# Performance work log

Measured on AMD Instinct MI355X. Metric: run time of the kernel, lower is better.

The kernel has to match this reference:

```python
import jax, jax.numpy as jnp
import numpy as np

N = 100_000      # nodes
E = 1_600_000    # edges
G = 256          # graphs in batch
FIN = 128


def setup_inputs() -> dict:
    key = jax.random.key(0)
    ks = jax.random.split(key, 12)
    inp = {
        "x": jax.random.normal(ks[0], (N, FIN), dtype=jnp.float32),
        "edge_index": jax.random.randint(ks[1], (2, E), 0, N),
        "batch": jnp.sort(jax.random.randint(ks[2], (N,), 0, G)),
    }
    def lin(k, fi, fo):
        return jax.random.normal(k, (fi, fo), dtype=jnp.float32) / np.sqrt(fi)
    inp["W1"], inp["b1"] = lin(ks[3], 128, 128), jnp.zeros((128,), jnp.float32)
    inp["W2"], inp["b2"] = lin(ks[4], 128, 128), jnp.zeros((128,), jnp.float32)
    inp["W3"], inp["b3"] = lin(ks[5], 128, 128), jnp.zeros((128,), jnp.float32)
    inp["Wa1"], inp["ba1"] = lin(ks[6], 128, 64), jnp.zeros((64,), jnp.float32)
    inp["Wa2"], inp["ba2"] = lin(ks[7], 64, 32), jnp.zeros((32,), jnp.float32)
    inp["Wa3"], inp["ba3"] = lin(ks[8], 32, 1), jnp.zeros((1,), jnp.float32)
    inp["Wm1"], inp["bm1"] = lin(ks[9], 128, 128), jnp.zeros((128,), jnp.float32)
    inp["Wm2"], inp["bm2"] = lin(ks[10], 128, 256), jnp.zeros((256,), jnp.float32)
    return inp


def _gcn_norm(edge_index, n):
    # PyG gcn_norm with added self-loops: D^{-1/2}(A+I)D^{-1/2}
    loops = jnp.arange(n)
    row = jnp.concatenate([edge_index[0], loops])
    col = jnp.concatenate([edge_index[1], loops])
    deg = jax.ops.segment_sum(jnp.ones_like(col, dtype=jnp.float32), col, n)
    dinv = jnp.where(deg > 0, jax.lax.rsqrt(jnp.maximum(deg, 1.0)), 0.0)
    return row, col, dinv[row] * dinv[col]


def _gcn(x, row, col, norm, W, b, n):
    h = x @ W                                   # linear first, then propagate
    out = jax.ops.segment_sum(h[row] * norm[:, None], col, n)
    return out + b


def _seg_softmax(w, batch, g):
    m = jax.ops.segment_max(w, batch, g)        # [G, 1]
    m = jnp.where(jnp.isfinite(m), m, 0.0)      # guard empty segments
    e = jnp.exp(w - m[batch])
    s = jax.ops.segment_sum(e, batch, g)
    return e / (s[batch] + 1e-16)


def reference(x, edge_index, batch, W1, b1, W2, b2, W3, b3,
              Wa1, ba1, Wa2, ba2, Wa3, ba3, Wm1, bm1, Wm2, bm2):
    n = x.shape[0]
    row, col, norm = _gcn_norm(edge_index, n)
    x = jax.nn.relu(_gcn(x, row, col, norm, W1, b1, n))
    x = jax.nn.relu(_gcn(x, row, col, norm, W2, b2, n))
    x = jax.nn.relu(_gcn(x, row, col, norm, W3, b3, n))
    w = jax.nn.relu(_gcn(x, row, col, norm, Wa1, ba1, n))
    w = jax.nn.relu(_gcn(w, row, col, norm, Wa2, ba2, n))
    w = jax.nn.relu(_gcn(w, row, col, norm, Wa3, ba3, n))  # [N, 1]
    w = _seg_softmax(w, batch, G)
    pooled = jax.ops.segment_sum(x * w, batch, G)           # [G, 128]
    h = jax.nn.relu(pooled @ Wm1 + bm1)
    return h @ Wm2 + bm2                                    # [G, 256]
```

## Files before the change

kernel.cpp:

```cpp
#include <hip/hip_runtime.h>
#include <hip/hip_bf16.h>

struct f4 { float x, y, z, w; };
__device__ __forceinline__ f4 ld4(const float* p) { return *(const f4*)p; }
__device__ __forceinline__ void st4(float* p, f4 v) { *(f4*)p = v; }
__device__ __forceinline__ void acc4(f4& a, f4 b) { a.x += b.x; a.y += b.y; a.z += b.z; a.w += b.w; }


__global__ void count_kernel(const int* __restrict__ col, int* __restrict__ cnt, int E) {
    int i = blockIdx.x * 256 + threadIdx.x;
    int e0 = i * 4;
    if (e0 + 4 <= E) {
        int4 c = *(const int4*)(col + e0);
        atomicAdd(&cnt[c.x], 1);
        atomicAdd(&cnt[c.y], 1);
        atomicAdd(&cnt[c.z], 1);
        atomicAdd(&cnt[c.w], 1);
    } else {
        for (int e = e0; e < E; ++e) atomicAdd(&cnt[col[e]], 1);
    }
}


__global__ void scan1_kernel(const int* __restrict__ cnt, int* __restrict__ bsum, int n) {
    __shared__ int red[256];
    int t = threadIdx.x;
    int i = blockIdx.x * 256 + t;
    red[t] = (i < n) ? cnt[i] : 0;
    __syncthreads();
    for (int off = 128; off > 0; off >>= 1) {
        if (t < off) red[t] += red[t + off];
        __syncthreads();
    }
    if (t == 0) bsum[blockIdx.x] = red[0];
}

__global__ void scan2_kernel(int* __restrict__ bsum, int nb) {
    __shared__ int s[1024];
    int t = threadIdx.x;
    int v = (t < nb) ? bsum[t] : 0;
    s[t] = v;
    __syncthreads();
    for (int off = 1; off < 1024; off <<= 1) {
        int u = (t >= off) ? s[t - off] : 0;
        __syncthreads();
        s[t] += u;
        __syncthreads();
    }
    if (t < nb) bsum[t] = s[t] - v;
}

__global__ void scan3_kernel(const int* __restrict__ cnt, const int* __restrict__ bsum,
                             int* __restrict__ ptr, int n) {
    __shared__ int s[256];
    int t = threadIdx.x;
    int i = blockIdx.x * 256 + t;
    int v = (i < n) ? cnt[i] : 0;
    s[t] = v;
    __syncthreads();
    for (int off = 1; off < 256; off <<= 1) {
        int u = (t >= off) ? s[t - off] : 0;
        __syncthreads();
        s[t] += u;
        __syncthreads();
    }
    int excl = s[t] - v + bsum[blockIdx.x];
    if (i < n) ptr[i] = excl;
    if (i == n - 1) ptr[n] = excl + v;
}

__global__ void dinv_fill_kernel(const int* __restrict__ cnt, const int* __restrict__ ptr,
                                 float* __restrict__ dinv, int* __restrict__ fillp, int n) {
    int i = blockIdx.x * 256 + threadIdx.x;
    if (i >= n) return;
    dinv[i] = rsqrtf((float)(cnt[i] + 1));
    fillp[i] = ptr[i];
}

__global__ void fill_kernel(const int* __restrict__ row, const int* __restrict__ col,
                            int* __restrict__ fillp, int* __restrict__ csr_row, int E) {
    int i = blockIdx.x * 256 + threadIdx.x;
    int e0 = i * 4;
    if (e0 + 4 <= E) {
        int4 c = *(const int4*)(col + e0);
        int4 r = *(const int4*)(row + e0);
        int p0 = atomicAdd(&fillp[c.x], 1);
        int p1 = atomicAdd(&fillp[c.y], 1);
        int p2 = atomicAdd(&fillp[c.z], 1);
        int p3 = atomicAdd(&fillp[c.w], 1);
        csr_row[p0] = r.x; csr_row[p1] = r.y; csr_row[p2] = r.z; csr_row[p3] = r.w;
    } else {
        for (int e = e0; e < E; ++e) {
            int p = atomicAdd(&fillp[col[e]], 1);
            csr_row[p] = row[e];
        }
    }
}


template<int K, int FOUT>
__global__ __launch_bounds__(256) void gemm_kernel(const float* __restrict__ A,
                            const float* __restrict__ W, const float* __restrict__ scale,
                            float* __restrict__ C, int n) {
    constexpr int ROWS = 64;
    constexpr int NCG = FOUT / 4;
    constexpr int RG  = 256 / NCG;
    constexpr int RPT = ROWS / RG;
    __shared__ float As[ROWS * K];
    int t = threadIdx.x;
    int r0 = blockIdx.x * ROWS;
    for (int i = t; i < ROWS * K / 4; i += 256) {
        int idx = i * 4;
        int r = r0 + idx / K;
        f4 v;
        if (r < n) v = ld4(A + (size_t)r0 * K + idx);
        else { v.x = v.y = v.z = v.w = 0.f; }
        st4(As + idx, v);
    }
    __syncthreads();
    int cg = t % NCG, rg = t / NCG;
    int c = cg * 4, rb = rg * RPT;
    f4 acc[RPT];
#pragma unroll
    for (int i = 0; i < RPT; ++i) { acc[i].x = acc[i].y = acc[i].z = acc[i].w = 0.f; }
    for (int k = 0; k < K; k += 4) {
        f4 w0 = ld4(W + (size_t)(k + 0) * FOUT + c);
        f4 w1 = ld4(W + (size_t)(k + 1) * FOUT + c);
        f4 w2 = ld4(W + (size_t)(k + 2) * FOUT + c);
        f4 w3 = ld4(W + (size_t)(k + 3) * FOUT + c);
#pragma unroll
        for (int i = 0; i < RPT; ++i) {
            f4 a = ld4(As + (rb + i) * K + k);
            acc[i].x += a.x * w0.x + a.y * w1.x + a.z * w2.x + a.w * w3.x;
            acc[i].y += a.x * w0.y + a.y * w1.y + a.z * w2.y + a.w * w3.y;
            acc[i].z += a.x * w0.z + a.y * w1.z + a.z * w2.z + a.w * w3.z;
            acc[i].w += a.x * w0.w + a.y * w1.w + a.z * w2.w + a.w * w3.w;
        }
    }
#pragma unroll
    for (int i = 0; i < RPT; ++i) {
        int r = r0 + rb + i;
        if (r < n) {
            float s = scale[r];
            f4 v = acc[i];
            v.x *= s; v.y *= s; v.z *= s; v.w *= s;
            st4(C + (size_t)r * FOUT + c, v);
        }
    }
}


template<int K, int FOUT, bool WRITE_AGG>
__global__ __launch_bounds__(512, 4) void propgemm_kernel(const float* __restrict__ Hs,
                            const int* __restrict__ ptr, const int* __restrict__ rows,
                            const float* __restrict__ dinv, const float* __restrict__ bias,
                            const float* __restrict__ W, float* __restrict__ aggout,
                            float* __restrict__ C, int n) {
    constexpr int ROWS = 64;
    constexpr int BT = 512;
    __shared__ float As[ROWS * K];
    int t = threadIdx.x;
    int r0 = blockIdx.x * ROWS;

    constexpr int L = K / 4;
    constexpr int NPB = BT / L;
    int q = t % L, ln = t / L;
    const int f4i = q * 4;
    for (int p = 0; p < ROWS; p += NPB) {
        int node = r0 + p + ln;
        f4 a0;
        if (node < n) {
            a0 = ld4(Hs + (size_t)node * K + f4i);
            f4 a1, a2, a3;
            a1.x = a1.y = a1.z = a1.w = 0.f; a2 = a1; a3 = a1;
            int e0 = ptr[node], e1 = ptr[node + 1];
            int e = e0;
            for (; e + 4 <= e1; e += 4) {
                int rr0 = rows[e], rr1 = rows[e+1], rr2 = rows[e+2], rr3 = rows[e+3];
                acc4(a0, ld4(Hs + (size_t)rr0 * K + f4i));
                acc4(a1, ld4(Hs + (size_t)rr1 * K + f4i));
                acc4(a2, ld4(Hs + (size_t)rr2 * K + f4i));
                acc4(a3, ld4(Hs + (size_t)rr3 * K + f4i));
            }
            for (; e < e1; ++e) acc4(a0, ld4(Hs + (size_t)rows[e] * K + f4i));
            acc4(a0, a1); acc4(a2, a3); acc4(a0, a2);
            float dn = dinv[node];
            f4 b = ld4(bias + f4i);
            a0.x = fmaxf(a0.x * dn + b.x, 0.f);
            a0.y = fmaxf(a0.y * dn + b.y, 0.f);
            a0.z = fmaxf(a0.z * dn + b.z, 0.f);
            a0.w = fmaxf(a0.w * dn + b.w, 0.f);
            if (WRITE_AGG) st4(aggout + (size_t)node * K + f4i, a0);
        } else { a0.x = a0.y = a0.z = a0.w = 0.f; }
        st4(As + (p + ln) * K + f4i, a0);
    }
    __syncthreads();

    constexpr int NCG = FOUT / 4;
    constexpr int RG  = BT / NCG;
    constexpr int RPT = ROWS / RG;
    int cg = t % NCG, rg = t / NCG;
    int c = cg * 4, rb = rg * RPT;
    f4 acc[RPT];
#pragma unroll
    for (int i = 0; i < RPT; ++i) { acc[i].x = acc[i].y = acc[i].z = acc[i].w = 0.f; }
    for (int k = 0; k < K; k += 4) {
        f4 w0 = ld4(W + (size_t)(k + 0) * FOUT + c);
        f4 w1 = ld4(W + (size_t)(k + 1) * FOUT + c);
        f4 w2 = ld4(W + (size_t)(k + 2) * FOUT + c);
        f4 w3 = ld4(W + (size_t)(k + 3) * FOUT + c);
#pragma unroll
        for (int i = 0; i < RPT; ++i) {
            f4 a = ld4(As + (rb + i) * K + k);
            acc[i].x += a.x * w0.x + a.y * w1.x + a.z * w2.x + a.w * w3.x;
            acc[i].y += a.x * w0.y + a.y * w1.y + a.z * w2.y + a.w * w3.y;
            acc[i].z += a.x * w0.z + a.y * w1.z + a.z * w2.z + a.w * w3.z;
            acc[i].w += a.x * w0.w + a.y * w1.w + a.z * w2.w + a.w * w3.w;
        }
    }
#pragma unroll
    for (int i = 0; i < RPT; ++i) {
        int r = r0 + rb + i;
        if (r < n) {
            float s = dinv[r];
            f4 v = acc[i];
            v.x *= s; v.y *= s; v.z *= s; v.w *= s;
            st4(C + (size_t)r * FOUT + c, v);
        }
    }
}


__global__ __launch_bounds__(256) void propdot_kernel(const float* __restrict__ Hs,
                            const int* __restrict__ ptr, const int* __restrict__ rows,
                            const float* __restrict__ dinv, const float* __restrict__ bias,
                            const float* __restrict__ W, float* __restrict__ outv, int n) {
    int t = threadIdx.x;
    int q = t & 7;
    int ln = t >> 3;
    int node = blockIdx.x * 32 + ln;
    if (node >= n) return;
    const int f4i = q * 4;
    f4 a0 = ld4(Hs + (size_t)node * 32 + f4i);
    f4 a1, a2, a3;
    a1.x = a1.y = a1.z = a1.w = 0.f; a2 = a1; a3 = a1;
    int e0 = ptr[node], e1 = ptr[node + 1];
    int e = e0;
    for (; e + 4 <= e1; e += 4) {
        int rr0 = rows[e], rr1 = rows[e+1], rr2 = rows[e+2], rr3 = rows[e+3];
        acc4(a0, ld4(Hs + (size_t)rr0 * 32 + f4i));
        acc4(a1, ld4(Hs + (size_t)rr1 * 32 + f4i));
        acc4(a2, ld4(Hs + (size_t)rr2 * 32 + f4i));
        acc4(a3, ld4(Hs + (size_t)rr3 * 32 + f4i));
    }
    for (; e < e1; ++e) acc4(a0, ld4(Hs + (size_t)rows[e] * 32 + f4i));
    acc4(a0, a1); acc4(a2, a3); acc4(a0, a2);
    float dn = dinv[node];
    f4 b = ld4(bias + f4i);
    float vx = fmaxf(a0.x * dn + b.x, 0.f);
    float vy = fmaxf(a0.y * dn + b.y, 0.f);
    float vz = fmaxf(a0.z * dn + b.z, 0.f);
    float vw = fmaxf(a0.w * dn + b.w, 0.f);
    f4 w = ld4(W + f4i);
    float part = vx * w.x + vy * w.y + vz * w.z + vw * w.w;
    part += __shfl_down(part, 4, 8);
    part += __shfl_down(part, 2, 8);
    part += __shfl_down(part, 1, 8);
    if (q == 0) outv[node] = part * dn;
}

__global__ void prop1_kernel(const float* __restrict__ Hs, const int* __restrict__ ptr,
                             const int* __restrict__ rows, const float* __restrict__ dinv,
                             const float* __restrict__ bias, float* __restrict__ out, int n) {
    int node = blockIdx.x * 256 + threadIdx.x;
    if (node >= n) return;
    float a0 = Hs[node], a1 = 0.f, a2 = 0.f, a3 = 0.f;
    int e0 = ptr[node], e1 = ptr[node + 1];
    int e = e0;
    for (; e + 4 <= e1; e += 4) {
        a0 += Hs[rows[e]];
        a1 += Hs[rows[e+1]];
        a2 += Hs[rows[e+2]];
        a3 += Hs[rows[e+3]];
    }
    for (; e < e1; ++e) a0 += Hs[rows[e]];
    float v = (a0 + a1 + a2 + a3) * dinv[node] + bias[0];
    out[node] = v > 0.f ? v : 0.f;
}


__global__ void bounds_kernel(const int* __restrict__ batch, int* __restrict__ start,
                              int n, int g_cnt) {
    int g = blockIdx.x * 256 + threadIdx.x;
    if (g > g_cnt) return;
    if (g == g_cnt) { start[g] = n; return; }
    int lo = 0, hi = n;
    while (lo < hi) { int mid = (lo + hi) >> 1; if (batch[mid] < g) lo = mid + 1; else hi = mid; }
    start[g] = lo;
}

__global__ __launch_bounds__(256) void softpool_kernel(const float* __restrict__ x,
                              const float* __restrict__ w, const int* __restrict__ start,
                              float* __restrict__ pooled) {
    int g = blockIdx.x;
    int s = start[g], e = start[g + 1];
    int t = threadIdx.x;
    __shared__ float red[256];
    float mx = -1e30f;
    for (int i = s + t; i < e; i += 256) mx = fmaxf(mx, w[i]);
    red[t] = mx; __syncthreads();
    for (int off = 128; off > 0; off >>= 1) {
        if (t < off) red[t] = fmaxf(red[t], red[t + off]);
        __syncthreads();
    }
    float m = (e > s) ? red[0] : 0.f;
    __syncthreads();
    float sm = 0.f;
    for (int i = s + t; i < e; i += 256) sm += expf(w[i] - m);
    red[t] = sm; __syncthreads();
    for (int off = 128; off > 0; off >>= 1) {
        if (t < off) red[t] += red[t + off];
        __syncthreads();
    }
    float denom = red[0] + 1e-16f;
    __syncthreads();
    int f = t & 127;
    int half = t >> 7;
    float acc = 0.f;
    for (int i = s + half; i < e; i += 2)
        acc += x[(size_t)i * 128 + f] * (expf(w[i] - m) / denom);
    red[t] = acc; __syncthreads();
    if (half == 0) pooled[g * 128 + f] = red[f] + red[128 + f];
}


__global__ void mlp1_kernel(const float* __restrict__ pooled, const float* __restrict__ Wm1,
                            const float* __restrict__ bm1, float* __restrict__ hidden) {
    int g = blockIdx.x, j = threadIdx.x;
    __shared__ float p[128];
    p[j] = pooled[g * 128 + j];
    __syncthreads();
    float acc = bm1[j];
    for (int k = 0; k < 128; ++k) acc += p[k] * Wm1[k * 128 + j];
    hidden[g * 128 + j] = acc > 0.f ? acc : 0.f;
}

__global__ void mlp2_kernel(const float* __restrict__ hidden, const float* __restrict__ Wm2,
                            const float* __restrict__ bm2, float* __restrict__ out) {
    int g = blockIdx.x, j = threadIdx.x;
    __shared__ float h[128];
    if (j < 128) h[j] = hidden[g * 128 + j];
    __syncthreads();
    float acc = bm2[j];
    for (int k = 0; k < 128; ++k) acc += h[k] * Wm2[k * 256 + j];
    out[g * 256 + j] = acc;
}


extern "C" void kernel_launch(void* const* d_in, const int* in_sizes, int n_in,
                              void* d_out, int out_size, void* d_ws, size_t ws_size,
                              hipStream_t stream) {
    const float* x    = (const float*)d_in[0];
    const int*   ei   = (const int*)d_in[1];
    const int*   batch= (const int*)d_in[2];
    const float* W1 = (const float*)d_in[3];  const float* b1 = (const float*)d_in[4];
    const float* W2 = (const float*)d_in[5];  const float* b2 = (const float*)d_in[6];
    const float* W3 = (const float*)d_in[7];  const float* b3 = (const float*)d_in[8];
    const float* Wa1= (const float*)d_in[9];  const float* ba1= (const float*)d_in[10];
    const float* Wa2= (const float*)d_in[11]; const float* ba2= (const float*)d_in[12];
    const float* Wa3= (const float*)d_in[13]; const float* ba3= (const float*)d_in[14];
    const float* Wm1= (const float*)d_in[15]; const float* bm1= (const float*)d_in[16];
    const float* Wm2= (const float*)d_in[17]; const float* bm2= (const float*)d_in[18];
    float* out = (float*)d_out;

    const int N = in_sizes[0] / 128;
    const int E = in_sizes[1] / 2;
    const int G = out_size / 256;

    const int* row = ei;
    const int* col = ei + E;

    char* wp = (char*)d_ws;
    auto alloc = [&](size_t bytes) {
        void* p = wp;
        wp += (bytes + 255) & ~(size_t)255;
        return p;
    };
    const int NB256 = (N + 255) / 256;
    int*   cnt     = (int*)alloc((size_t)N * 4);
    int*   ptr     = (int*)alloc((size_t)(N + 1) * 4);
    int*   bsum    = (int*)alloc((size_t)NB256 * 4);
    int*   fillp   = (int*)alloc((size_t)N * 4);
    int*   csr_row = (int*)alloc((size_t)E * 4);
    float* dinv    = (float*)alloc((size_t)N * 4);
    float* bufA    = (float*)alloc((size_t)N * 128 * 4);
    float* bufB    = (float*)alloc((size_t)N * 128 * 4);
    float* a64_lin = (float*)alloc((size_t)N * 64 * 4);
    float* a32_lin = (float*)alloc((size_t)N * 32 * 4);
    float* wb0     = (float*)alloc((size_t)N * 4);
    float* wb1     = (float*)alloc((size_t)N * 4);
    int*   gstart  = (int*)alloc((size_t)(G + 1) * 4);
    float* pooled  = (float*)alloc((size_t)G * 128 * 4);
    float* hidden  = (float*)alloc((size_t)G * 128 * 4);

    hipMemsetAsync(cnt, 0, (size_t)N * 4, stream);

    const int E4B = ((E + 3) / 4 + 255) / 256;
    const int NB = NB256;

    count_kernel<<<E4B, 256, 0, stream>>>(col, cnt, E);
    scan1_kernel<<<NB, 256, 0, stream>>>(cnt, bsum, N);
    scan2_kernel<<<1, 1024, 0, stream>>>(bsum, NB);
    scan3_kernel<<<NB, 256, 0, stream>>>(cnt, bsum, ptr, N);
    dinv_fill_kernel<<<NB, 256, 0, stream>>>(cnt, ptr, dinv, fillp, N);
    fill_kernel<<<E4B, 256, 0, stream>>>(row, col, fillp, csr_row, E);
    bounds_kernel<<<(G + 256) / 256, 256, 0, stream>>>(batch, gstart, N, G);

    const int GB64 = (N + 63) / 64;

    gemm_kernel<128,128><<<GB64, 256, 0, stream>>>(x, W1, dinv, bufA, N);
    propgemm_kernel<128,128,false><<<GB64, 512, 0, stream>>>(bufA, ptr, csr_row, dinv, b1, W2, nullptr, bufB, N);
    propgemm_kernel<128,128,false><<<GB64, 512, 0, stream>>>(bufB, ptr, csr_row, dinv, b2, W3, nullptr, bufA, N);
    propgemm_kernel<128,64,true><<<GB64, 512, 0, stream>>>(bufA, ptr, csr_row, dinv, b3, Wa1, bufB, a64_lin, N);
    propgemm_kernel<64,32,false><<<GB64, 512, 0, stream>>>(a64_lin, ptr, csr_row, dinv, ba1, Wa2, nullptr, a32_lin, N);
    propdot_kernel<<<(N + 31) / 32, 256, 0, stream>>>(a32_lin, ptr, csr_row, dinv, ba2, Wa3, wb0, N);
    prop1_kernel<<<NB, 256, 0, stream>>>(wb0, ptr, csr_row, dinv, ba3, wb1, N);

    softpool_kernel<<<G, 256, 0, stream>>>(bufB, wb1, gstart, pooled);

    mlp1_kernel<<<G, 128, 0, stream>>>(pooled, Wm1, bm1, hidden);
    mlp2_kernel<<<G, 256, 0, stream>>>(hidden, Wm2, bm2, out);
}
```

Measured before the change: 1.146 ms.

## Fuse scan with dinv init, merge MLP kernels, shrink propgemm blocks

Folds the dinv/fillp initialization into the final scan kernel and merges the two MLP head kernels into one, removing two launches and an intermediate buffer. The CSR fill now uses nontemporal stores for the scattered row writes. The propagate+GEMM kernels drop from 512 to 256 threads per block, which changes per-block aggregation parallelism and occupancy. Each block now has fewer threads to cover the same 64 rows, so each thread does more gather work.

```diff
diff --git a/kernel.cpp b/kernel.cpp
--- a/kernel.cpp
+++ b/kernel.cpp
@@ -50,8 +50,9 @@
     if (t < nb) bsum[t] = s[t] - v;
 }
 
-__global__ void scan3_kernel(const int* __restrict__ cnt, const int* __restrict__ bsum,
-                             int* __restrict__ ptr, int n) {
+__global__ void scan3_dinv_kernel(const int* __restrict__ cnt, const int* __restrict__ bsum,
+                                  int* __restrict__ ptr, float* __restrict__ dinv,
+                                  int* __restrict__ fillp, int n) {
     __shared__ int s[256];
     int t = threadIdx.x;
     int i = blockIdx.x * 256 + t;
@@ -65,16 +66,12 @@
         __syncthreads();
     }
     int excl = s[t] - v + bsum[blockIdx.x];
-    if (i < n) ptr[i] = excl;
+    if (i < n) {
+        ptr[i] = excl;
+        fillp[i] = excl;
+        dinv[i] = rsqrtf((float)(v + 1));
+    }
     if (i == n - 1) ptr[n] = excl + v;
-}
-
-__global__ void dinv_fill_kernel(const int* __restrict__ cnt, const int* __restrict__ ptr,
-                                 float* __restrict__ dinv, int* __restrict__ fillp, int n) {
-    int i = blockIdx.x * 256 + threadIdx.x;
-    if (i >= n) return;
-    dinv[i] = rsqrtf((float)(cnt[i] + 1));
-    fillp[i] = ptr[i];
 }
 
 __global__ void fill_kernel(const int* __restrict__ row, const int* __restrict__ col,
@@ -88,11 +85,14 @@
         int p1 = atomicAdd(&fillp[c.y], 1);
         int p2 = atomicAdd(&fillp[c.z], 1);
         int p3 = atomicAdd(&fillp[c.w], 1);
-        csr_row[p0] = r.x; csr_row[p1] = r.y; csr_row[p2] = r.z; csr_row[p3] = r.w;
+        __builtin_nontemporal_store(r.x, csr_row + p0);
+        __builtin_nontemporal_store(r.y, csr_row + p1);
+        __builtin_nontemporal_store(r.z, csr_row + p2);
+        __builtin_nontemporal_store(r.w, csr_row + p3);
     } else {
         for (int e = e0; e < E; ++e) {
             int p = atomicAdd(&fillp[col[e]], 1);
-            csr_row[p] = row[e];
+            __builtin_nontemporal_store(row[e], csr_row + p);
         }
     }
 }
@@ -151,13 +151,13 @@
 
 
 template<int K, int FOUT, bool WRITE_AGG>
-__global__ __launch_bounds__(512, 4) void propgemm_kernel(const float* __restrict__ Hs,
+__global__ __launch_bounds__(256) void propgemm_kernel(const float* __restrict__ Hs,
                             const int* __restrict__ ptr, const int* __restrict__ rows,
                             const float* __restrict__ dinv, const float* __restrict__ bias,
                             const float* __restrict__ W, float* __restrict__ aggout,
                             float* __restrict__ C, int n) {
     constexpr int ROWS = 64;
-    constexpr int BT = 512;
+    constexpr int BT = 256;
     __shared__ float As[ROWS * K];
     int t = threadIdx.x;
     int r0 = blockIdx.x * ROWS;
@@ -334,22 +334,19 @@
 }
 
 
-__global__ void mlp1_kernel(const float* __restrict__ pooled, const float* __restrict__ Wm1,
-                            const float* __restrict__ bm1, float* __restrict__ hidden) {
+__global__ __launch_bounds__(256) void mlp_kernel(const float* __restrict__ pooled,
+                            const float* __restrict__ Wm1, const float* __restrict__ bm1,
+                            const float* __restrict__ Wm2, const float* __restrict__ bm2,
+                            float* __restrict__ out) {
     int g = blockIdx.x, j = threadIdx.x;
-    __shared__ float p[128];
-    p[j] = pooled[g * 128 + j];
-    __syncthreads();
-    float acc = bm1[j];
-    for (int k = 0; k < 128; ++k) acc += p[k] * Wm1[k * 128 + j];
-    hidden[g * 128 + j] = acc > 0.f ? acc : 0.f;
-}
-
-__global__ void mlp2_kernel(const float* __restrict__ hidden, const float* __restrict__ Wm2,
-                            const float* __restrict__ bm2, float* __restrict__ out) {
-    int g = blockIdx.x, j = threadIdx.x;
-    __shared__ float h[128];
-    if (j < 128) h[j] = hidden[g * 128 + j];
+    __shared__ float p[128], h[128];
+    if (j < 128) p[j] = pooled[g * 128 + j];
+    __syncthreads();
+    if (j < 128) {
+        float acc = bm1[j];
+        for (int k = 0; k < 128; ++k) acc += p[k] * Wm1[k * 128 + j];
+        h[j] = acc > 0.f ? acc : 0.f;
+    }
     __syncthreads();
     float acc = bm2[j];
     for (int k = 0; k < 128; ++k) acc += h[k] * Wm2[k * 256 + j];
@@ -401,7 +398,6 @@
     float* wb1     = (float*)alloc((size_t)N * 4);
     int*   gstart  = (int*)alloc((size_t)(G + 1) * 4);
     float* pooled  = (float*)alloc((size_t)G * 128 * 4);
-    float* hidden  = (float*)alloc((size_t)G * 128 * 4);
 
     hipMemsetAsync(cnt, 0, (size_t)N * 4, stream);
 
@@ -411,23 +407,21 @@
     count_kernel<<<E4B, 256, 0, stream>>>(col, cnt, E);
     scan1_kernel<<<NB, 256, 0, stream>>>(cnt, bsum, N);
     scan2_kernel<<<1, 1024, 0, stream>>>(bsum, NB);
-    scan3_kernel<<<NB, 256, 0, stream>>>(cnt, bsum, ptr, N);
-    dinv_fill_kernel<<<NB, 256, 0, stream>>>(cnt, ptr, dinv, fillp, N);
+    scan3_dinv_kernel<<<NB, 256, 0, stream>>>(cnt, bsum, ptr, dinv, fillp, N);
     fill_kernel<<<E4B, 256, 0, stream>>>(row, col, fillp, csr_row, E);
     bounds_kernel<<<(G + 256) / 256, 256, 0, stream>>>(batch, gstart, N, G);
 
     const int GB64 = (N + 63) / 64;
 
     gemm_kernel<128,128><<<GB64, 256, 0, stream>>>(x, W1, dinv, bufA, N);
-    propgemm_kernel<128,128,false><<<GB64, 512, 0, stream>>>(bufA, ptr, csr_row, dinv, b1, W2, nullptr, bufB, N);
-    propgemm_kernel<128,128,false><<<GB64, 512, 0, stream>>>(bufB, ptr, csr_row, dinv, b2, W3, nullptr, bufA, N);
-    propgemm_kernel<128,64,true><<<GB64, 512, 0, stream>>>(bufA, ptr, csr_row, dinv, b3, Wa1, bufB, a64_lin, N);
-    propgemm_kernel<64,32,false><<<GB64, 512, 0, stream>>>(a64_lin, ptr, csr_row, dinv, ba1, Wa2, nullptr, a32_lin, N);
+    propgemm_kernel<128,128,false><<<GB64, 256, 0, stream>>>(bufA, ptr, csr_row, dinv, b1, W2, nullptr, bufB, N);
+    propgemm_kernel<128,128,false><<<GB64, 256, 0, stream>>>(bufB, ptr, csr_row, dinv, b2, W3, nullptr, bufA, N);
+    propgemm_kernel<128,64,true><<<GB64, 256, 0, stream>>>(bufA, ptr, csr_row, dinv, b3, Wa1, bufB, a64_lin, N);
+    propgemm_kernel<64,32,false><<<GB64, 256, 0, stream>>>(a64_lin, ptr, csr_row, dinv, ba1, Wa2, nullptr, a32_lin, N);
     propdot_kernel<<<(N + 31) / 32, 256, 0, stream>>>(a32_lin, ptr, csr_row, dinv, ba2, Wa3, wb0, N);
     prop1_kernel<<<NB, 256, 0, stream>>>(wb0, ptr, csr_row, dinv, ba3, wb1, N);
 
     softpool_kernel<<<G, 256, 0, stream>>>(bufB, wb1, gstart, pooled);
 
-    mlp1_kernel<<<G, 128, 0, stream>>>(pooled, Wm1, bm1, hidden);
-    mlp2_kernel<<<G, 256, 0, stream>>>(hidden, Wm2, bm2, out);
-}
+    mlp_kernel<<<G, 256, 0, stream>>>(pooled, Wm1, bm1, Wm2, bm2, out);
+}
```

New measurement: 1.132 ms. Within noise of the previous version (-1.2%).
